# Kernel optimization log

Hardware: AMD Instinct MI355X
Metric: run time of the kernel (lower is better)

The kernel has to match this reference:

```python
import jax, jax.numpy as jnp
import numpy as np

BATCH = 8192
IN_CH = 64          # input_channels
CH = 256            # output channels per row
BOARD = 27          # board_edge**3
EDGE = 3
ROWS = 49           # 3*(board_edge+1)**2 + 1


def _wincon_mats():
    # Faithful port of init_wincon_matrix(); returns (27, 3, 49) 0/1 matrix.
    step = [0]
    mats = np.zeros((BOARD, EDGE, ROWS), dtype=np.float32)
    col = 0
    x = y = z = 0

    def put():
        mats[x + 3 * y + 9 * z, step[0], col] = 1
        step[0] = (step[0] + 1) % 3

    for x in range(3):
        for y in range(3):
            for z in range(3):
                put()
            col += 1
        for z in range(3):
            for y in range(3):
                put()
            col += 1
        for y in range(3):
            z = y
            put()
        col += 1
        for y in range(3):
            z = 2 - y
            put()
        col += 1
    for z in range(3):
        for y in range(3):
            for x in range(3):
                put()
            col += 1
        for y in range(3):
            x = y
            put()
        col += 1
        for y in range(3):
            x = 2 - y
            put()
        col += 1
    for y in range(3):
        for z in range(3):
            x = z
            put()
        col += 1
        for z in range(3):
            x = 2 - z
            put()
        col += 1
    for x in range(3):
        y = z = x
        put()
    col += 1
    for x in range(3):
        y = z = 2 - x
        put()
    col += 1
    for x in range(3):
        y = x
        z = 2 - x
        put()
    col += 1
    for x in range(3):
        z = x
        y = 2 - x
        put()
    col += 1
    return mats


_MATS = jnp.asarray(_wincon_mats())  # (board_size=27, edge=3, row_count=49)


def setup_inputs() -> dict:
    key = jax.random.key(0)
    k1, k2, k3 = jax.random.split(key, 3)
    x = jax.random.normal(k1, (BATCH, IN_CH * BOARD), dtype=jnp.float32)
    # keras 'random_normal' initializer: stddev 0.05
    v = jax.random.normal(k2, (EDGE, IN_CH, ROWS, CH), dtype=jnp.float32) * 0.05
    b = jax.random.normal(k3, (CH * ROWS,), dtype=jnp.float32) * 0.05
    return {"x": x, "v": v, "b": b}


def reference(x, v, b):
    # Weight synthesis: w[bd, i, r, c] = sum_e mats[bd, e, r] * v[e, i, r, c]
    # (same math as the broadcast+multiply+reduce in the original, fused via einsum)
    w = jnp.einsum('ber,eirc->birc', _MATS, v)            # (27, in_ch, 49, ch)
    w = w.reshape(BOARD * IN_CH, ROWS * CH)              # (1728, 12544)
    return x @ w + b
```

## Files before the change

kernel.cpp:

```cpp
#include <hip/hip_runtime.h>
#include <cstdint>
#include <cstddef>


#define XCOLS   1728
#define ROWS_W  49
#define KTOT    192
#define OUTW    12544

typedef __attribute__((ext_vector_type(8))) short short8;
typedef __attribute__((ext_vector_type(4))) float f32x4;

struct CellTab { int c[ROWS_W][3]; };

constexpr CellTab make_cells() {
    CellTab t{};
    int step = 0, col = 0;
    int x = 0, y = 0, z = 0;
#define PUT() do { t.c[col][step] = x + 3*y + 9*z; step = (step + 1) % 3; } while (0)
    for (x = 0; x < 3; ++x) {
        for (y = 0; y < 3; ++y) {
            for (z = 0; z < 3; ++z) PUT();
            ++col;
        }
        for (z = 0; z < 3; ++z) {
            for (y = 0; y < 3; ++y) PUT();
            ++col;
        }
        for (y = 0; y < 3; ++y) { z = y; PUT(); }
        ++col;
        for (y = 0; y < 3; ++y) { z = 2 - y; PUT(); }
        ++col;
    }
    for (z = 0; z < 3; ++z) {
        for (y = 0; y < 3; ++y) {
            for (x = 0; x < 3; ++x) PUT();
            ++col;
        }
        for (y = 0; y < 3; ++y) { x = y; PUT(); }
        ++col;
        for (y = 0; y < 3; ++y) { x = 2 - y; PUT(); }
        ++col;
    }
    for (y = 0; y < 3; ++y) {
        for (z = 0; z < 3; ++z) { x = z; PUT(); }
        ++col;
        for (z = 0; z < 3; ++z) { x = 2 - z; PUT(); }
        ++col;
    }
    for (x = 0; x < 3; ++x) { y = x; z = x; PUT(); }
    ++col;
    for (x = 0; x < 3; ++x) { y = 2 - x; z = 2 - x; PUT(); }
    ++col;
    for (x = 0; x < 3; ++x) { y = x; z = 2 - x; PUT(); }
    ++col;
    for (x = 0; x < 3; ++x) { z = x; y = 2 - x; PUT(); }
    ++col;
#undef PUT
    return t;
}

__constant__ CellTab CELLS = make_cells();

__device__ __forceinline__ unsigned short f2bf(float f) {
    union { float f; unsigned u; } a; a.f = f;
    unsigned u = a.u;
    return (unsigned short)((u + 0x7fffu + ((u >> 16) & 1u)) >> 16);
}

__global__ __launch_bounds__(256) void wt_prepass(const float* __restrict__ v,
                                                  unsigned short* __restrict__ wt) {
    const int kq = blockIdx.x;
    const int r  = blockIdx.y;
    const int c  = threadIdx.x;
    const int k0 = kq * 32;
    unsigned short tmp[32];
#pragma unroll
    for (int kk = 0; kk < 32; ++kk) {
        const int k = k0 + kk;
        tmp[kk] = f2bf(v[(size_t)(k * 49 + r) * 256 + c]);
    }
    unsigned short* dst = wt + (size_t)(r * 256 + c) * KTOT + k0;
#pragma unroll
    for (int j = 0; j < 4; ++j) {
        short8 s;
#pragma unroll
        for (int i = 0; i < 8; ++i) s[i] = (short)tmp[j * 8 + i];
        *(short8*)(dst + j * 8) = s;
    }
}

__global__ __launch_bounds__(256, 2) void tic_gemm(
    const float* __restrict__ x,
    const unsigned short* __restrict__ wt,
    const float* __restrict__ bias,
    float* __restrict__ out)
{
    const int bid   = blockIdx.x;
    const int r     = bid >> 7;
    const int sub   = bid & 127;
    const int mbase = (sub >> 1) * 128;
    const int cbase = (sub & 1) * 128;

    const int t    = threadIdx.x;
    const int wave = t >> 6;
    const int lane = t & 63;
    const int l15  = lane & 15;
    const int quad = lane >> 4;

    __shared__ __align__(16) unsigned short Bs[2][4096];

    const int cell0 = CELLS.c[r][0];
    const int cell1 = CELLS.c[r][1];
    const int cell2 = CELLS.c[r][2];
    const int cells[3] = { cell0, cell1, cell2 };

    f32x4 acc[2][8];
#pragma unroll
    for (int nt = 0; nt < 8; ++nt) {
        const float bv = bias[r * 256 + cbase + nt * 16 + l15];
        f32x4 a; a[0] = bv; a[1] = bv; a[2] = bv; a[3] = bv;
        acc[0][nt] = a; acc[1][nt] = a;
    }

    auto stageB = [&](int kc, int buf) {
#pragma unroll
        for (int q = 0; q < 2; ++q) {
            const int cb = q * 256 + wave * 64;
            const int g  = cb >> 7;
            const int n  = (cb & 127) + lane;
            const unsigned short* src =
                wt + (size_t)(r * 256 + cbase + n) * KTOT + kc * 32 + g * 8;
            unsigned short* dst = &Bs[buf][cb * 8];
            __builtin_amdgcn_global_load_lds(
                (const __attribute__((address_space(1))) unsigned int*)src,
                (__attribute__((address_space(3))) unsigned int*)dst,
                16, 0, 0);
        }
    };

    float afp[2][2][8];
    auto loadA = [&](int kc, int parity) {
        const int e = kc >> 1, h = kc & 1;
        const int colb = cells[e] * 64 + h * 32 + quad * 8;
#pragma unroll
        for (int mt = 0; mt < 2; ++mt) {
            const int row = mbase + wave * 32 + mt * 16 + l15;
            const float* p = x + (size_t)row * XCOLS + colb;
            const float4 a0 = *(const float4*)p;
            const float4 a1 = *(const float4*)(p + 4);
            afp[parity][mt][0] = a0.x; afp[parity][mt][1] = a0.y;
            afp[parity][mt][2] = a0.z; afp[parity][mt][3] = a0.w;
            afp[parity][mt][4] = a1.x; afp[parity][mt][5] = a1.y;
            afp[parity][mt][6] = a1.z; afp[parity][mt][7] = a1.w;
        }
    };

    loadA(0, 0);
    stageB(0, 0);
    __syncthreads();

#pragma unroll
    for (int kc = 0; kc < 6; ++kc) {
        const int buf = kc & 1;
        if (kc < 5) {
            stageB(kc + 1, buf ^ 1);
            loadA(kc + 1, (kc + 1) & 1);
        }
        short8 afr[2];
#pragma unroll
        for (int mt = 0; mt < 2; ++mt) {
            short8 a;
#pragma unroll
            for (int j = 0; j < 8; ++j) a[j] = (short)f2bf(afp[kc & 1][mt][j]);
            afr[mt] = a;
        }
#pragma unroll
        for (int nt = 0; nt < 8; ++nt) {
            const short8 bfr = *(const short8*)&Bs[buf][(quad * 128 + nt * 16 + l15) * 8];
            acc[0][nt] = __builtin_amdgcn_mfma_f32_16x16x32_bf16(afr[0], bfr, acc[0][nt], 0, 0, 0);
            acc[1][nt] = __builtin_amdgcn_mfma_f32_16x16x32_bf16(afr[1], bfr, acc[1][nt], 0, 0, 0);
        }
        __syncthreads();
    }

#pragma unroll
    for (int mt = 0; mt < 2; ++mt) {
#pragma unroll
        for (int v4 = 0; v4 < 4; ++v4) {
            const int row = mbase + wave * 32 + mt * 16 + quad * 4 + v4;
            float* orow = out + (size_t)row * OUTW + r * 256 + cbase;
#pragma unroll
            for (int nt = 0; nt < 8; ++nt)
                orow[nt * 16 + l15] = acc[mt][nt][v4];
        }
    }
}

extern "C" void kernel_launch(void* const* d_in, const int* in_sizes, int n_in,
                              void* d_out, int out_size, void* d_ws, size_t ws_size,
                              hipStream_t stream) {
    const float* x  = (const float*)d_in[0];
    const float* v  = (const float*)d_in[1];
    const float* b  = (const float*)d_in[2];
    float* out = (float*)d_out;
    unsigned short* wt = (unsigned short*)d_ws;

    wt_prepass<<<dim3(6, 49), dim3(256), 0, stream>>>(v, wt);
    tic_gemm<<<dim3(49 * 128), dim3(256), 0, stream>>>(x, wt, b, out);
}
```

Before: 547.8 us.

## Pre-convert x to bf16 and widen GEMM tile to full 256 columns

Adds a prepass that converts x to bf16 in the workspace, so the GEMM loads half the bytes per A fragment and skips per-tile conversion. Each block now covers a 128x256 output tile (4 M-tiles per wave, two waves per column half) instead of 128x128, which halves the redundant A reads. Blocks are reordered so the 49 row groups for one M-block are adjacent. The costs are an extra full pass over x (read fp32, write bf16), more accumulator registers and twice the LDS per block, which could lower occupancy.

After: 535.0 us. -2.3%, faster.

```diff
diff --git a/kernel.cpp b/kernel.cpp
--- a/kernel.cpp
+++ b/kernel.cpp
@@ -7,6 +7,7 @@
 #define ROWS_W  49
 #define KTOT    192
 #define OUTW    12544
+#define XELEMS  (8192 * XCOLS)
 
 typedef __attribute__((ext_vector_type(8))) short short8;
 typedef __attribute__((ext_vector_type(4))) float f32x4;
@@ -68,6 +69,19 @@
     return (unsigned short)((u + 0x7fffu + ((u >> 16) & 1u)) >> 16);
 }
 
+__global__ __launch_bounds__(256) void x_prepass(const float* __restrict__ x,
+                                                 unsigned short* __restrict__ xb) {
+    const size_t i8 = (size_t)(blockIdx.x * 256 + threadIdx.x) * 8;
+    const float4 a0 = *(const float4*)(x + i8);
+    const float4 a1 = *(const float4*)(x + i8 + 4);
+    short8 s;
+    s[0] = (short)f2bf(a0.x); s[1] = (short)f2bf(a0.y);
+    s[2] = (short)f2bf(a0.z); s[3] = (short)f2bf(a0.w);
+    s[4] = (short)f2bf(a1.x); s[5] = (short)f2bf(a1.y);
+    s[6] = (short)f2bf(a1.z); s[7] = (short)f2bf(a1.w);
+    *(short8*)(xb + i8) = s;
+}
+
 __global__ __launch_bounds__(256) void wt_prepass(const float* __restrict__ v,
                                                   unsigned short* __restrict__ wt) {
     const int kq = blockIdx.x;
@@ -91,46 +105,44 @@
 }
 
 __global__ __launch_bounds__(256, 2) void tic_gemm(
-    const float* __restrict__ x,
+    const unsigned short* __restrict__ xb,
     const unsigned short* __restrict__ wt,
     const float* __restrict__ bias,
     float* __restrict__ out)
 {
     const int bid   = blockIdx.x;
-    const int r     = bid >> 7;
-    const int sub   = bid & 127;
-    const int mbase = (sub >> 1) * 128;
-    const int cbase = (sub & 1) * 128;
+    const int m     = bid / 49;
+    const int r     = bid % 49;
+    const int mbase = m * 128;
 
     const int t    = threadIdx.x;
     const int wave = t >> 6;
     const int lane = t & 63;
     const int l15  = lane & 15;
     const int quad = lane >> 4;
-
-    __shared__ __align__(16) unsigned short Bs[2][4096];
-
-    const int cell0 = CELLS.c[r][0];
-    const int cell1 = CELLS.c[r][1];
-    const int cell2 = CELLS.c[r][2];
-    const int cells[3] = { cell0, cell1, cell2 };
-
-    f32x4 acc[2][8];
+    const int half = wave & 1;
+    const int wh   = wave >> 1;
+
+    __shared__ __align__(16) unsigned short Bs[2][8192];
+
+    const int cells[3] = { CELLS.c[r][0], CELLS.c[r][1], CELLS.c[r][2] };
+
+    f32x4 acc[4][8];
 #pragma unroll
     for (int nt = 0; nt < 8; ++nt) {
-        const float bv = bias[r * 256 + cbase + nt * 16 + l15];
+        const float bv = bias[r * 256 + half * 128 + nt * 16 + l15];
         f32x4 a; a[0] = bv; a[1] = bv; a[2] = bv; a[3] = bv;
-        acc[0][nt] = a; acc[1][nt] = a;
+#pragma unroll
+        for (int mt = 0; mt < 4; ++mt) acc[mt][nt] = a;
     }
 
     auto stageB = [&](int kc, int buf) {
 #pragma unroll
-        for (int q = 0; q < 2; ++q) {
+        for (int q = 0; q < 4; ++q) {
             const int cb = q * 256 + wave * 64;
-            const int g  = cb >> 7;
-            const int n  = (cb & 127) + lane;
+            const int n  = wave * 64 + lane;
             const unsigned short* src =
-                wt + (size_t)(r * 256 + cbase + n) * KTOT + kc * 32 + g * 8;
+                wt + (size_t)(r * 256 + n) * KTOT + kc * 32 + q * 8;
             unsigned short* dst = &Bs[buf][cb * 8];
             __builtin_amdgcn_global_load_lds(
                 (const __attribute__((address_space(1))) unsigned int*)src,
@@ -139,20 +151,14 @@
         }
     };
 
-    float afp[2][2][8];
+    short8 afr[2][4];
     auto loadA = [&](int kc, int parity) {
         const int e = kc >> 1, h = kc & 1;
         const int colb = cells[e] * 64 + h * 32 + quad * 8;
 #pragma unroll
-        for (int mt = 0; mt < 2; ++mt) {
-            const int row = mbase + wave * 32 + mt * 16 + l15;
-            const float* p = x + (size_t)row * XCOLS + colb;
-            const float4 a0 = *(const float4*)p;
-            const float4 a1 = *(const float4*)(p + 4);
-            afp[parity][mt][0] = a0.x; afp[parity][mt][1] = a0.y;
-            afp[parity][mt][2] = a0.z; afp[parity][mt][3] = a0.w;
-            afp[parity][mt][4] = a1.x; afp[parity][mt][5] = a1.y;
-            afp[parity][mt][6] = a1.z; afp[parity][mt][7] = a1.w;
+        for (int mt = 0; mt < 4; ++mt) {
+            const int row = mbase + wh * 64 + mt * 16 + l15;
+            afr[parity][mt] = *(const short8*)(xb + (size_t)row * XCOLS + colb);
         }
     };
 
@@ -167,29 +173,24 @@
             stageB(kc + 1, buf ^ 1);
             loadA(kc + 1, (kc + 1) & 1);
         }
-        short8 afr[2];
-#pragma unroll
-        for (int mt = 0; mt < 2; ++mt) {
-            short8 a;
-#pragma unroll
-            for (int j = 0; j < 8; ++j) a[j] = (short)f2bf(afp[kc & 1][mt][j]);
-            afr[mt] = a;
-        }
 #pragma unroll
         for (int nt = 0; nt < 8; ++nt) {
-            const short8 bfr = *(const short8*)&Bs[buf][(quad * 128 + nt * 16 + l15) * 8];
-            acc[0][nt] = __builtin_amdgcn_mfma_f32_16x16x32_bf16(afr[0], bfr, acc[0][nt], 0, 0, 0);
-            acc[1][nt] = __builtin_amdgcn_mfma_f32_16x16x32_bf16(afr[1], bfr, acc[1][nt], 0, 0, 0);
+            const short8 bfr = *(const short8*)
+                &Bs[buf][(quad * 256 + half * 128 + nt * 16 + l15) * 8];
+#pragma unroll
+            for (int mt = 0; mt < 4; ++mt)
+                acc[mt][nt] = __builtin_amdgcn_mfma_f32_16x16x32_bf16(
+                    afr[kc & 1][mt], bfr, acc[mt][nt], 0, 0, 0);
         }
         __syncthreads();
     }
 
 #pragma unroll
-    for (int mt = 0; mt < 2; ++mt) {
+    for (int mt = 0; mt < 4; ++mt) {
 #pragma unroll
         for (int v4 = 0; v4 < 4; ++v4) {
-            const int row = mbase + wave * 32 + mt * 16 + quad * 4 + v4;
-            float* orow = out + (size_t)row * OUTW + r * 256 + cbase;
+            const int row = mbase + wh * 64 + mt * 16 + quad * 4 + v4;
+            float* orow = out + (size_t)row * OUTW + r * 256 + half * 128;
 #pragma unroll
             for (int nt = 0; nt < 8; ++nt)
                 orow[nt * 16 + l15] = acc[mt][nt][v4];
@@ -204,8 +205,11 @@
     const float* v  = (const float*)d_in[1];
     const float* b  = (const float*)d_in[2];
     float* out = (float*)d_out;
-    unsigned short* wt = (unsigned short*)d_ws;
-
+
+    unsigned short* xb = (unsigned short*)d_ws;
+    unsigned short* wt = xb + (size_t)XELEMS;
+
+    x_prepass<<<dim3(XELEMS / (256 * 8)), dim3(256), 0, stream>>>(x, xb);
     wt_prepass<<<dim3(6, 49), dim3(256), 0, stream>>>(v, wt);
-    tic_gemm<<<dim3(49 * 128), dim3(256), 0, stream>>>(x, wt, b, out);
-}
+    tic_gemm<<<dim3(64 * 49), dim3(256), 0, stream>>>(xb, wt, b, out);
+}
```
